# Kernel tuning notes

Measured on AMD Instinct MI355X. Metric: run time of the kernel, lower is better.

## Reference

```python
import jax, jax.numpy as jnp
import numpy as np

N_NODES = 100000
N_EDGES = 1600000
EDGE_FEAT = 16
EDGE_HID = 32
NODE_FEAT = 128


def setup_inputs() -> dict:
    key = jax.random.key(0)
    ks = jax.random.split(key, 10)
    inp = {
        "edge_logits": jax.random.normal(ks[0], (N_EDGES, 1), dtype=jnp.float32),
        "edge_feats": jax.random.normal(ks[1], (N_EDGES, EDGE_FEAT), dtype=jnp.float32),
        "node_feats": jax.random.normal(ks[2], (N_NODES, NODE_FEAT), dtype=jnp.float32),
        "dst": jax.random.randint(ks[3], (N_EDGES,), 0, N_NODES, dtype=jnp.int32),
        # edge_transform Linear(edge_feat -> edge_hid)
        "W_et": jax.random.normal(ks[4], (EDGE_FEAT, EDGE_HID), dtype=jnp.float32) * (1.0 / np.sqrt(EDGE_FEAT)),
        "b_et": jnp.zeros((EDGE_HID,), dtype=jnp.float32),
        # MLP Linear(edge_hid + node_feat -> node_feat)
        "W1": jax.random.normal(ks[5], (EDGE_HID + NODE_FEAT, NODE_FEAT), dtype=jnp.float32) * (1.0 / np.sqrt(EDGE_HID + NODE_FEAT)),
        "b1": jnp.zeros((NODE_FEAT,), dtype=jnp.float32),
        # MLP Linear(node_feat -> node_feat)
        "W2": jax.random.normal(ks[6], (NODE_FEAT, NODE_FEAT), dtype=jnp.float32) * (1.0 / np.sqrt(NODE_FEAT)),
        "b2": jnp.zeros((NODE_FEAT,), dtype=jnp.float32),
    }
    return inp


def reference(edge_logits, edge_feats, node_feats, dst, W_et, b_et, W1, b1, W2, b2):
    # edge_softmax: segment softmax of edge_logits grouped by destination node
    logits = edge_logits[:, 0]                                        # [E]
    seg_max = jax.ops.segment_max(logits, dst, num_segments=N_NODES)  # [N]
    seg_max = jnp.where(jnp.isfinite(seg_max), seg_max, 0.0)          # guard empty segments
    ex = jnp.exp(logits - seg_max[dst])                               # [E]
    denom = jax.ops.segment_sum(ex, dst, num_segments=N_NODES)        # [N]
    denom = jnp.where(denom == 0.0, 1.0, denom)
    alpha = ex / denom[dst]                                           # [E]
    # edge transform (dropout is identity in eval) then weight by attention
    e = alpha[:, None] * (edge_feats @ W_et + b_et)                   # [E, H]
    # scatter-sum aggregation to destination nodes
    c = jax.ops.segment_sum(e, dst, num_segments=N_NODES)             # [N, H]
    context = jax.nn.elu(c)
    h = jnp.concatenate([context, node_feats], axis=1)                # [N, H+F]
    h = jax.nn.relu(h @ W1 + b1)
    return jax.nn.relu(h @ W2 + b2)                                   # [N, F]
```

## Files before the change

kernel.cpp:

```cpp
#include <hip/hip_runtime.h>

#define EF 16
#define EH 32
#define NF 128
#define K1 160
#define HS 168
#define H2S 136

typedef __attribute__((ext_vector_type(8))) short bf16x8;
typedef __attribute__((ext_vector_type(4))) float f32x4;

__device__ __forceinline__ unsigned short f2b(float f) {
  unsigned u = __float_as_uint(f);
  u += 0x7FFFu + ((u >> 16) & 1u);
  return (unsigned short)(u >> 16);
}
__device__ __forceinline__ unsigned pack2b(float a, float b) {
  return (unsigned)f2b(a) | ((unsigned)f2b(b) << 16);
}

__global__ void k_init(unsigned* __restrict__ cnt, int n,
                       const float* __restrict__ W1, const float* __restrict__ W2,
                       unsigned short* __restrict__ w1t, unsigned short* __restrict__ w2t) {
  int i = blockIdx.x * blockDim.x + threadIdx.x;
  if (i < n) cnt[i] = 0u;
  if (i < K1 * NF) {
    int nn = i / K1, k = i % K1;
    w1t[i] = f2b(W1[k * NF + nn]);
  } else if (i < K1 * NF + NF * NF) {
    int j = i - K1 * NF;
    int nn = j / NF, k = j % NF;
    w2t[j] = f2b(W2[k * NF + nn]);
  }
}

__global__ void k_hist(const int* __restrict__ dst, unsigned* __restrict__ cnt,
                       unsigned* __restrict__ rank, int n_edges) {
  int e = blockIdx.x * blockDim.x + threadIdx.x;
  if (e >= n_edges) return;
  rank[e] = atomicAdd(&cnt[dst[e]], 1u);
}

__global__ void k_scan1(const unsigned* __restrict__ cnt, unsigned* __restrict__ offs,
                        unsigned* __restrict__ bsum, int n) {
  __shared__ unsigned ts[256];
  int t = threadIdx.x;
  int base = blockIdx.x * 1024 + t * 4;
  unsigned v[4];
#pragma unroll
  for (int i = 0; i < 4; ++i) { int idx = base + i; v[i] = (idx < n) ? cnt[idx] : 0u; }
  unsigned run = 0;
#pragma unroll
  for (int i = 0; i < 4; ++i) { unsigned x = v[i]; v[i] = run; run += x; }
  ts[t] = run;
  __syncthreads();
  for (int off = 1; off < 256; off <<= 1) {
    unsigned add = (t >= off) ? ts[t - off] : 0u;
    __syncthreads();
    ts[t] += add;
    __syncthreads();
  }
  unsigned texcl = (t > 0) ? ts[t - 1] : 0u;
  if (t == 255) bsum[blockIdx.x] = ts[255];
#pragma unroll
  for (int i = 0; i < 4; ++i) { int idx = base + i; if (idx < n) offs[idx] = v[i] + texcl; }
}

__global__ void k_scan3(unsigned* __restrict__ offs, const unsigned* __restrict__ bsum,
                        int n, int nb) {
  __shared__ unsigned ts[256];
  int t = threadIdx.x;
  ts[t] = (t < nb) ? bsum[t] : 0u;
  __syncthreads();
  for (int off = 1; off < 256; off <<= 1) {
    unsigned add = (t >= off) ? ts[t - off] : 0u;
    __syncthreads();
    ts[t] += add;
    __syncthreads();
  }
  unsigned add = (blockIdx.x > 0) ? ts[blockIdx.x - 1] : 0u;
  int base = blockIdx.x * 1024 + t * 4;
#pragma unroll
  for (int i = 0; i < 4; ++i) { int idx = base + i; if (idx < n) offs[idx] += add; }
}

__global__ void k_scatter(const int* __restrict__ dst, const unsigned* __restrict__ rank,
                          const float* __restrict__ logits, const unsigned* __restrict__ offs,
                          const float* __restrict__ efeat,
                          unsigned* __restrict__ prodb, float* __restrict__ exs, int n_edges) {
  int e = blockIdx.x * blockDim.x + threadIdx.x;
  if (e >= n_edges) return;
  int d = dst[e];
  unsigned slot = offs[d] + rank[e];
  float ex = __expf(logits[e]);
  exs[slot] = ex;
  const float4* fp = (const float4*)(efeat + (size_t)e * EF);
  float4 v0 = fp[0], v1 = fp[1], v2 = fp[2], v3 = fp[3];
  uint4 o0, o1;
  o0.x = pack2b(ex * v0.x, ex * v0.y);
  o0.y = pack2b(ex * v0.z, ex * v0.w);
  o0.z = pack2b(ex * v1.x, ex * v1.y);
  o0.w = pack2b(ex * v1.z, ex * v1.w);
  o1.x = pack2b(ex * v2.x, ex * v2.y);
  o1.y = pack2b(ex * v2.z, ex * v2.w);
  o1.z = pack2b(ex * v3.x, ex * v3.y);
  o1.w = pack2b(ex * v3.z, ex * v3.w);
  uint4* pp = (uint4*)(prodb + (size_t)slot * 8);
  pp[0] = o0;
  pp[1] = o1;
}

__global__ __launch_bounds__(256) void k_gather(
    const unsigned* __restrict__ prodb, const float* __restrict__ exs,
    const unsigned* __restrict__ cnt, const unsigned* __restrict__ offs,
    const float* __restrict__ W_et, const float* __restrict__ b_et,
    unsigned short* __restrict__ ctxb, int n_nodes) {
  int node = (int)((blockIdx.x * blockDim.x + threadIdx.x) >> 6);
  if (node >= n_nodes) return;
  int lane = threadIdx.x & 63;
  unsigned start = offs[node];
  unsigned deg = cnt[node];
  int rg = lane >> 3, c = lane & 7;
  float a0 = 0.0f, a1 = 0.0f;
  for (unsigned i = rg; i < deg; i += 8) {
    unsigned p = prodb[(size_t)(start + i) * 8 + c];
    a0 += __uint_as_float(p << 16);
    a1 += __uint_as_float(p & 0xFFFF0000u);
  }
  a0 += __shfl_xor(a0, 8);  a1 += __shfl_xor(a1, 8);
  a0 += __shfl_xor(a0, 16); a1 += __shfl_xor(a1, 16);
  a0 += __shfl_xor(a0, 32); a1 += __shfl_xor(a1, 32);
  float dsum = 0.0f;
  for (unsigned i = lane; i < deg; i += 64) dsum += exs[start + i];
  dsum += __shfl_xor(dsum, 1);
  dsum += __shfl_xor(dsum, 2);
  dsum += __shfl_xor(dsum, 4);
  dsum += __shfl_xor(dsum, 8);
  dsum += __shfl_xor(dsum, 16);
  dsum += __shfl_xor(dsum, 32);
  float inv = (deg > 0) ? 1.0f / dsum : 0.0f;
  float S = (deg > 0) ? 1.0f : 0.0f;
  int j = lane & 31;
  float acc = 0.0f;
#pragma unroll
  for (int k = 0; k < 16; ++k) {
    float sk = (k & 1) ? __shfl(a1, k >> 1) : __shfl(a0, k >> 1);
    acc += sk * W_et[k * EH + j];
  }
  float cv = acc * inv + S * b_et[j];
  float ctxv = (cv > 0.0f) ? cv : (__expf(cv) - 1.0f);
  if (lane < 32) ctxb[(size_t)node * EH + lane] = f2b(ctxv);
}

__global__ __launch_bounds__(256) void k_node(
    const unsigned short* __restrict__ ctxb, const float* __restrict__ nf,
    const unsigned short* __restrict__ w1t, const unsigned short* __restrict__ w2t,
    const float* __restrict__ b1, const float* __restrict__ b2,
    float* __restrict__ out, int n_nodes) {
  __shared__ __align__(16) unsigned short hA[64 * HS];
  __shared__ __align__(16) unsigned short hB[64 * H2S];
  const int t = threadIdx.x;
  const int w = t >> 6, lane = t & 63;
  const int m = lane & 15, q = lane >> 4;
  int n0 = blockIdx.x * 64;
  if (n0 + 64 > n_nodes) n0 = n_nodes - 64;

  {
    int node = t >> 2, j = (t & 3) * 8;
    *(uint4*)&hA[node * HS + j] = *(const uint4*)&ctxb[(size_t)(n0 + node) * EH + j];
  }
#pragma unroll
  for (int i = 0; i < 8; ++i) {
    int idx = t + 256 * i;
    int node = idx >> 5, j = (idx & 31) * 4;
    float4 v = *(const float4*)&nf[(size_t)(n0 + node) * NF + j];
    unsigned short r[4] = {f2b(v.x), f2b(v.y), f2b(v.z), f2b(v.w)};
    *(uint2*)&hA[node * HS + EH + j] = *(const uint2*)r;
  }
  __syncthreads();

  const int mr = w * 16;
  f32x4 acc[8];
#pragma unroll
  for (int nt = 0; nt < 8; ++nt) acc[nt] = (f32x4){0.f, 0.f, 0.f, 0.f};
  for (int ks = 0; ks < 5; ++ks) {
    bf16x8 a = *(const bf16x8*)&hA[(mr + m) * HS + ks * 32 + q * 8];
#pragma unroll
    for (int nt = 0; nt < 8; ++nt) {
      bf16x8 b = *(const bf16x8*)&w1t[(size_t)(nt * 16 + m) * K1 + ks * 32 + q * 8];
      acc[nt] = __builtin_amdgcn_mfma_f32_16x16x32_bf16(a, b, acc[nt], 0, 0, 0);
    }
  }
#pragma unroll
  for (int nt = 0; nt < 8; ++nt) {
    float bb = b1[nt * 16 + m];
#pragma unroll
    for (int r = 0; r < 4; ++r) {
      float v = fmaxf(acc[nt][r] + bb, 0.0f);
      hB[(mr + q * 4 + r) * H2S + nt * 16 + m] = f2b(v);
    }
  }
  __syncthreads();

  f32x4 ac2[8];
#pragma unroll
  for (int nt = 0; nt < 8; ++nt) ac2[nt] = (f32x4){0.f, 0.f, 0.f, 0.f};
  for (int ks = 0; ks < 4; ++ks) {
    bf16x8 a = *(const bf16x8*)&hB[(mr + m) * H2S + ks * 32 + q * 8];
#pragma unroll
    for (int nt = 0; nt < 8; ++nt) {
      bf16x8 b = *(const bf16x8*)&w2t[(size_t)(nt * 16 + m) * NF + ks * 32 + q * 8];
      ac2[nt] = __builtin_amdgcn_mfma_f32_16x16x32_bf16(a, b, ac2[nt], 0, 0, 0);
    }
  }
#pragma unroll
  for (int nt = 0; nt < 8; ++nt) {
    float bb = b2[nt * 16 + m];
#pragma unroll
    for (int r = 0; r < 4; ++r) {
      out[(size_t)(n0 + mr + q * 4 + r) * NF + nt * 16 + m] = fmaxf(ac2[nt][r] + bb, 0.0f);
    }
  }
}

extern "C" void kernel_launch(void* const* d_in, const int* in_sizes, int n_in,
                              void* d_out, int out_size, void* d_ws, size_t ws_size,
                              hipStream_t stream) {
  const float* edge_logits = (const float*)d_in[0];
  const float* edge_feats  = (const float*)d_in[1];
  const float* node_feats  = (const float*)d_in[2];
  const int*   dst         = (const int*)d_in[3];
  const float* W_et        = (const float*)d_in[4];
  const float* b_et        = (const float*)d_in[5];
  const float* W1          = (const float*)d_in[6];
  const float* b1          = (const float*)d_in[7];
  const float* W2          = (const float*)d_in[8];
  const float* b2          = (const float*)d_in[9];
  float* out = (float*)d_out;

  const int E = in_sizes[0];
  const int n = in_sizes[2] / NF;

  unsigned* cnt   = (unsigned*)d_ws;
  unsigned* offs  = cnt + n;
  unsigned* bsum  = offs + n;
  unsigned* rank  = bsum + 256;
  float*    exs   = (float*)(rank + E);
  unsigned* prodb = (unsigned*)(exs + E);
  unsigned short* ctxb = (unsigned short*)(prodb + (size_t)E * 8);
  unsigned short* w1t  = ctxb + (size_t)n * EH;
  unsigned short* w2t  = w1t + NF * K1;

  const int thr = 256;
  const int nscan = (n + 1023) / 1024;

  k_init<<<(n + thr - 1) / thr, thr, 0, stream>>>(cnt, n, W1, W2, w1t, w2t);
  k_hist<<<(E + thr - 1) / thr, thr, 0, stream>>>(dst, cnt, rank, E);
  k_scan1<<<nscan, 256, 0, stream>>>(cnt, offs, bsum, n);
  k_scan3<<<nscan, 256, 0, stream>>>(offs, bsum, n, nscan);
  k_scatter<<<(E + thr - 1) / thr, thr, 0, stream>>>(dst, rank, edge_logits, offs, edge_feats,
                                                     prodb, exs, E);
  k_gather<<<(n * 64 + thr - 1) / thr, thr, 0, stream>>>(prodb, exs, cnt, offs,
                                                         W_et, b_et, ctxb, n);
  k_node<<<(n + 63) / 64, 256, 0, stream>>>(ctxb, node_feats, w1t, w2t, b1, b2, out, n);
}
```

Measured before the change: 429.8 us.

## Replace per-node counting sort with coarse bucket binning and LDS atomic accumulation

The per-node histogram, two-level scan and rank-based scatter are replaced by a bucket sort over groups of 128 destination nodes: a block-local LDS histogram over 782 buckets, a single-block scan, and binning through global atomic tails. Each bucket is then reduced by one block that accumulates the weighted edge features and softmax denominators with shared-memory float atomics, and then applies W_et and ELU. This drops the per-node atomics, the rank array and the large scan, but adds contended global atomics on the bucket tails, LDS atomic contention, and hardcoded NBUCK/1024-bucket limits tied to the node count.

```diff
diff --git a/kernel.cpp b/kernel.cpp
--- a/kernel.cpp
+++ b/kernel.cpp
@@ -6,6 +6,9 @@
 #define K1 160
 #define HS 168
 #define H2S 136
+#define BSH 7
+#define BNODES 128
+#define NBUCK 782
 
 typedef __attribute__((ext_vector_type(8))) short bf16x8;
 typedef __attribute__((ext_vector_type(4))) float f32x4;
@@ -19,11 +22,11 @@
   return (unsigned)f2b(a) | ((unsigned)f2b(b) << 16);
 }
 
-__global__ void k_init(unsigned* __restrict__ cnt, int n,
+__global__ void k_init(unsigned* __restrict__ bcnt,
                        const float* __restrict__ W1, const float* __restrict__ W2,
                        unsigned short* __restrict__ w1t, unsigned short* __restrict__ w2t) {
   int i = blockIdx.x * blockDim.x + threadIdx.x;
-  if (i < n) cnt[i] = 0u;
+  if (i < 1024) bcnt[i] = 0u;
   if (i < K1 * NF) {
     int nn = i / K1, k = i % K1;
     w1t[i] = f2b(W1[k * NF + nn]);
@@ -34,21 +37,34 @@
   }
 }
 
-__global__ void k_hist(const int* __restrict__ dst, unsigned* __restrict__ cnt,
-                       unsigned* __restrict__ rank, int n_edges) {
-  int e = blockIdx.x * blockDim.x + threadIdx.x;
-  if (e >= n_edges) return;
-  rank[e] = atomicAdd(&cnt[dst[e]], 1u);
-}
-
-__global__ void k_scan1(const unsigned* __restrict__ cnt, unsigned* __restrict__ offs,
-                        unsigned* __restrict__ bsum, int n) {
+__global__ __launch_bounds__(256) void k_bcount(const int* __restrict__ dst,
+                                                unsigned* __restrict__ bcnt, int E) {
+  __shared__ unsigned lh[NBUCK];
+  int t = threadIdx.x;
+  for (int i = t; i < NBUCK; i += 256) lh[i] = 0u;
+  __syncthreads();
+  int base = blockIdx.x * 4096;
+#pragma unroll
+  for (int i = 0; i < 16; ++i) {
+    int e = base + t + 256 * i;
+    if (e < E) atomicAdd(&lh[((unsigned)dst[e]) >> BSH], 1u);
+  }
+  __syncthreads();
+  for (int i = t; i < NBUCK; i += 256) {
+    unsigned c = lh[i];
+    if (c) atomicAdd(&bcnt[i], c);
+  }
+}
+
+__global__ __launch_bounds__(256) void k_bscan(const unsigned* __restrict__ bcnt,
+                                               unsigned* __restrict__ bbase,
+                                               unsigned* __restrict__ tails) {
   __shared__ unsigned ts[256];
   int t = threadIdx.x;
-  int base = blockIdx.x * 1024 + t * 4;
+  int base = t * 4;
   unsigned v[4];
 #pragma unroll
-  for (int i = 0; i < 4; ++i) { int idx = base + i; v[i] = (idx < n) ? cnt[idx] : 0u; }
+  for (int i = 0; i < 4; ++i) { int idx = base + i; v[i] = (idx < NBUCK) ? bcnt[idx] : 0u; }
   unsigned run = 0;
 #pragma unroll
   for (int i = 0; i < 4; ++i) { unsigned x = v[i]; v[i] = run; run += x; }
@@ -61,39 +77,29 @@
     __syncthreads();
   }
   unsigned texcl = (t > 0) ? ts[t - 1] : 0u;
-  if (t == 255) bsum[blockIdx.x] = ts[255];
-#pragma unroll
-  for (int i = 0; i < 4; ++i) { int idx = base + i; if (idx < n) offs[idx] = v[i] + texcl; }
-}
-
-__global__ void k_scan3(unsigned* __restrict__ offs, const unsigned* __restrict__ bsum,
-                        int n, int nb) {
-  __shared__ unsigned ts[256];
-  int t = threadIdx.x;
-  ts[t] = (t < nb) ? bsum[t] : 0u;
-  __syncthreads();
-  for (int off = 1; off < 256; off <<= 1) {
-    unsigned add = (t >= off) ? ts[t - off] : 0u;
-    __syncthreads();
-    ts[t] += add;
-    __syncthreads();
-  }
-  unsigned add = (blockIdx.x > 0) ? ts[blockIdx.x - 1] : 0u;
-  int base = blockIdx.x * 1024 + t * 4;
-#pragma unroll
-  for (int i = 0; i < 4; ++i) { int idx = base + i; if (idx < n) offs[idx] += add; }
-}
-
-__global__ void k_scatter(const int* __restrict__ dst, const unsigned* __restrict__ rank,
-                          const float* __restrict__ logits, const unsigned* __restrict__ offs,
-                          const float* __restrict__ efeat,
-                          unsigned* __restrict__ prodb, float* __restrict__ exs, int n_edges) {
-  int e = blockIdx.x * blockDim.x + threadIdx.x;
-  if (e >= n_edges) return;
-  int d = dst[e];
-  unsigned slot = offs[d] + rank[e];
+#pragma unroll
+  for (int i = 0; i < 4; ++i) {
+    int idx = base + i;
+    if (idx < NBUCK) { unsigned o = v[i] + texcl; bbase[idx] = o; tails[idx] = o; }
+  }
+}
+
+__global__ __launch_bounds__(256) void k_bin(const int* __restrict__ dst,
+                                             const float* __restrict__ logits,
+                                             const float* __restrict__ efeat,
+                                             unsigned* __restrict__ tails,
+                                             uint2* __restrict__ meta,
+                                             unsigned* __restrict__ prodb, int E) {
+  int e = blockIdx.x * 256 + threadIdx.x;
+  if (e >= E) return;
+  unsigned d = (unsigned)dst[e];
+  unsigned b = d >> BSH;
   float ex = __expf(logits[e]);
-  exs[slot] = ex;
+  unsigned slot = atomicAdd(&tails[b], 1u);
+  uint2 mv;
+  mv.x = d & (BNODES - 1);
+  mv.y = __float_as_uint(ex);
+  meta[slot] = mv;
   const float4* fp = (const float4*)(efeat + (size_t)e * EF);
   float4 v0 = fp[0], v1 = fp[1], v2 = fp[2], v3 = fp[3];
   uint4 o0, o1;
@@ -110,46 +116,56 @@
   pp[1] = o1;
 }
 
-__global__ __launch_bounds__(256) void k_gather(
-    const unsigned* __restrict__ prodb, const float* __restrict__ exs,
-    const unsigned* __restrict__ cnt, const unsigned* __restrict__ offs,
+__global__ __launch_bounds__(256) void k_accum(
+    const unsigned* __restrict__ prodb, const uint2* __restrict__ meta,
+    const unsigned* __restrict__ bcnt, const unsigned* __restrict__ bbase,
     const float* __restrict__ W_et, const float* __restrict__ b_et,
     unsigned short* __restrict__ ctxb, int n_nodes) {
-  int node = (int)((blockIdx.x * blockDim.x + threadIdx.x) >> 6);
-  if (node >= n_nodes) return;
-  int lane = threadIdx.x & 63;
-  unsigned start = offs[node];
-  unsigned deg = cnt[node];
-  int rg = lane >> 3, c = lane & 7;
-  float a0 = 0.0f, a1 = 0.0f;
-  for (unsigned i = rg; i < deg; i += 8) {
-    unsigned p = prodb[(size_t)(start + i) * 8 + c];
-    a0 += __uint_as_float(p << 16);
-    a1 += __uint_as_float(p & 0xFFFF0000u);
-  }
-  a0 += __shfl_xor(a0, 8);  a1 += __shfl_xor(a1, 8);
-  a0 += __shfl_xor(a0, 16); a1 += __shfl_xor(a1, 16);
-  a0 += __shfl_xor(a0, 32); a1 += __shfl_xor(a1, 32);
-  float dsum = 0.0f;
-  for (unsigned i = lane; i < deg; i += 64) dsum += exs[start + i];
-  dsum += __shfl_xor(dsum, 1);
-  dsum += __shfl_xor(dsum, 2);
-  dsum += __shfl_xor(dsum, 4);
-  dsum += __shfl_xor(dsum, 8);
-  dsum += __shfl_xor(dsum, 16);
-  dsum += __shfl_xor(dsum, 32);
-  float inv = (deg > 0) ? 1.0f / dsum : 0.0f;
-  float S = (deg > 0) ? 1.0f : 0.0f;
-  int j = lane & 31;
-  float acc = 0.0f;
-#pragma unroll
-  for (int k = 0; k < 16; ++k) {
-    float sk = (k & 1) ? __shfl(a1, k >> 1) : __shfl(a0, k >> 1);
-    acc += sk * W_et[k * EH + j];
-  }
-  float cv = acc * inv + S * b_et[j];
-  float ctxv = (cv > 0.0f) ? cv : (__expf(cv) - 1.0f);
-  if (lane < 32) ctxb[(size_t)node * EH + lane] = f2b(ctxv);
+  __shared__ float s[BNODES * 17];
+  const int t = threadIdx.x;
+  const int b = blockIdx.x;
+  for (int i = t; i < BNODES * 17; i += 256) s[i] = 0.0f;
+  __syncthreads();
+  const unsigned cnt = bcnt[b];
+  const unsigned base = bbase[b];
+  for (unsigned i = t; i < cnt; i += 256) {
+    uint2 mv = meta[base + i];
+    float* sp = &s[mv.x * 17];
+    float ex = __uint_as_float(mv.y);
+    const uint4* pp = (const uint4*)(prodb + (size_t)(base + i) * 8);
+    uint4 p0 = pp[0], p1 = pp[1];
+    unsigned pv[8] = {p0.x, p0.y, p0.z, p0.w, p1.x, p1.y, p1.z, p1.w};
+#pragma unroll
+    for (int k = 0; k < 8; ++k) {
+      atomicAdd(sp + 2 * k,     __uint_as_float(pv[k] << 16));
+      atomicAdd(sp + 2 * k + 1, __uint_as_float(pv[k] & 0xFFFF0000u));
+    }
+    atomicAdd(sp + 16, ex);
+  }
+  __syncthreads();
+  int nd = t >> 1;
+  int node = b * BNODES + nd;
+  if (node < n_nodes) {
+    float dsum = s[nd * 17 + 16];
+    bool nz = (dsum != 0.0f);
+    float inv = nz ? 1.0f / dsum : 0.0f;
+    float S = nz ? 1.0f : 0.0f;
+    int j0 = (t & 1) * 16;
+    unsigned short obuf[16];
+#pragma unroll
+    for (int jj = 0; jj < 16; ++jj) {
+      int j = j0 + jj;
+      float acc = 0.0f;
+#pragma unroll
+      for (int k = 0; k < 16; ++k) acc += s[nd * 17 + k] * W_et[k * EH + j];
+      float cv = acc * inv + S * b_et[j];
+      float cx = (cv > 0.0f) ? cv : (__expf(cv) - 1.0f);
+      obuf[jj] = f2b(cx);
+    }
+    uint4* op = (uint4*)&ctxb[(size_t)node * EH + j0];
+    op[0] = *(const uint4*)&obuf[0];
+    op[1] = *(const uint4*)&obuf[8];
+  }
 }
 
 __global__ __launch_bounds__(256) void k_node(
@@ -241,26 +257,22 @@
   const int E = in_sizes[0];
   const int n = in_sizes[2] / NF;
 
-  unsigned* cnt   = (unsigned*)d_ws;
-  unsigned* offs  = cnt + n;
-  unsigned* bsum  = offs + n;
-  unsigned* rank  = bsum + 256;
-  float*    exs   = (float*)(rank + E);
-  unsigned* prodb = (unsigned*)(exs + E);
+  unsigned* bcnt  = (unsigned*)d_ws;
+  unsigned* bbase = bcnt + 1024;
+  unsigned* tails = bbase + 1024;
+  uint2*    meta  = (uint2*)(tails + 1024);
+  unsigned* prodb = (unsigned*)(meta + E);
   unsigned short* ctxb = (unsigned short*)(prodb + (size_t)E * 8);
   unsigned short* w1t  = ctxb + (size_t)n * EH;
   unsigned short* w2t  = w1t + NF * K1;
 
   const int thr = 256;
-  const int nscan = (n + 1023) / 1024;
-
-  k_init<<<(n + thr - 1) / thr, thr, 0, stream>>>(cnt, n, W1, W2, w1t, w2t);
-  k_hist<<<(E + thr - 1) / thr, thr, 0, stream>>>(dst, cnt, rank, E);
-  k_scan1<<<nscan, 256, 0, stream>>>(cnt, offs, bsum, n);
-  k_scan3<<<nscan, 256, 0, stream>>>(offs, bsum, n, nscan);
-  k_scatter<<<(E + thr - 1) / thr, thr, 0, stream>>>(dst, rank, edge_logits, offs, edge_feats,
-                                                     prodb, exs, E);
-  k_gather<<<(n * 64 + thr - 1) / thr, thr, 0, stream>>>(prodb, exs, cnt, offs,
-                                                         W_et, b_et, ctxb, n);
-  k_node<<<(n + 63) / 64, 256, 0, stream>>>(ctxb, node_feats, w1t, w2t, b1, b2, out, n);
-}
+
+  k_init<<<(K1 * NF + NF * NF + thr - 1) / thr, thr, 0, stream>>>(bcnt, W1, W2, w1t, w2t);
+  k_bcount<<<(E + 4095) / 4096, thr, 0, stream>>>(dst, bcnt, E);
+  k_bscan<<<1, thr, 0, stream>>>(bcnt, bbase, tails);
+  k_bin<<<(E + thr - 1) / thr, thr, 0, stream>>>(dst, edge_logits, edge_feats, tails,
+                                                 meta, prodb, E);
+  k_accum<<<NBUCK, thr, 0, stream>>>(prodb, meta, bcnt, bbase, W_et, b_et, ctxb, n);
+  k_node<<<(n + 63) / 64, thr, 0, stream>>>(ctxb, node_feats, w1t, w2t, b1, b2, out, n);
+}
```

After: 800.8 us. 1.86x slower.
